# Optimization experiments

Hardware: AMD Instinct MI355X
Metric: run time of the kernel (lower is better)

The kernel has to match this reference:

```python
import jax, jax.numpy as jnp
import numpy as np

BATCH, SEQ, D_IN, D_HID, N_CLS = 256, 128, 1024, 2048, 1024


def setup_inputs() -> dict:
    key = jax.random.key(0)
    ks = jax.random.split(key, 6)
    s_in = 1.0 / np.sqrt(D_IN)
    s_hid = 1.0 / np.sqrt(D_HID)
    return {
        "x": jax.random.normal(ks[0], (BATCH, SEQ, D_IN), dtype=jnp.float32),
        "W_hx": jax.random.normal(ks[1], (D_HID, D_IN), dtype=jnp.float32) * s_in,
        "W_hh": jax.random.normal(ks[2], (D_HID, D_HID), dtype=jnp.float32) * s_hid,
        "W_ph": jax.random.normal(ks[3], (N_CLS, D_HID), dtype=jnp.float32) * s_hid,
        "b_h": jax.random.normal(ks[4], (D_HID,), dtype=jnp.float32) * 0.01,
        "b_p": jax.random.normal(ks[5], (N_CLS,), dtype=jnp.float32) * 0.01,
    }


def reference(x, W_hx, W_hh, W_ph, b_h, b_p):
    # Input projection for all timesteps in one large GEMM: [B,S,Din] @ [Din,H] -> [B,S,H]
    xproj = jnp.einsum("bsd,hd->bsh", x, W_hx) + b_h  # bias folded in once per step
    h0 = jnp.zeros((x.shape[0], W_hh.shape[0]), dtype=x.dtype)

    def step(h_prev, xp_t):
        # h_t = W_hx x_t + W_hh h_prev + b_h (linear recurrence, as in source)
        h_t = xp_t + h_prev @ W_hh.T
        return h_t, None

    # scan over time axis: xproj transposed to [S,B,H]
    h_T, _ = jax.lax.scan(step, h0, jnp.swapaxes(xproj, 0, 1))
    # readout from final hidden state: p = W_ph h_T + b_p -> [B, C]
    p = h_T @ W_ph.T + b_p
    return p
```

## Files before the change

### kernel.cpp

```cpp
#include <hip/hip_runtime.h>
#include <stdint.h>

#define B_SZ   256
#define SEQ_LEN 128
#define DIN    1024
#define DHID   2048
#define NCLS   1024
#define NBLK   256
#define NROUND 8

typedef unsigned short ushort_t;
typedef short bf16x8 __attribute__((ext_vector_type(8)));
typedef float f32x16 __attribute__((ext_vector_type(16)));

__device__ __forceinline__ ushort_t f32_to_bf16(float f) {
  uint32_t u = __builtin_bit_cast(uint32_t, f);
  u = (u + 0x7FFFu + ((u >> 16) & 1u)) >> 16;
  return (ushort_t)u;
}
__device__ __forceinline__ float bf16_to_f32(ushort_t h) {
  uint32_t u = ((uint32_t)h) << 16;
  return __builtin_bit_cast(float, u);
}

__device__ __forceinline__ void llds16(const ushort_t* g, ushort_t* l) {
  __builtin_amdgcn_global_load_lds(
      (const __attribute__((address_space(1))) void*)g,
      (__attribute__((address_space(3))) void*)l, 16, 0, 0);
}

__device__ __forceinline__ void cstore_f32(float* p, float v) {
  __hip_atomic_store(p, v, __ATOMIC_RELAXED, __HIP_MEMORY_SCOPE_AGENT);
}
__device__ __forceinline__ void cstore_u64(void* p, uint64_t v) {
  __hip_atomic_store((uint64_t*)p, v, __ATOMIC_RELAXED, __HIP_MEMORY_SCOPE_AGENT);
}
__device__ __forceinline__ uint64_t cload_u64(const void* p) {
  return __hip_atomic_load((const uint64_t*)p, __ATOMIC_RELAXED, __HIP_MEMORY_SCOPE_AGENT);
}
__device__ __forceinline__ void cstore_u32(unsigned* p, unsigned v) {
  __hip_atomic_store(p, v, __ATOMIC_RELAXED, __HIP_MEMORY_SCOPE_AGENT);
}
__device__ __forceinline__ unsigned cload_u32(const unsigned* p) {
  return __hip_atomic_load(p, __ATOMIC_RELAXED, __HIP_MEMORY_SCOPE_AGENT);
}

__device__ __forceinline__ void gsync(unsigned* flags, unsigned ep) {
  __syncthreads();
  if (threadIdx.x == 0) cstore_u32(&flags[blockIdx.x], ep);
  if (threadIdx.x < 64) {
    const unsigned* f = flags + threadIdx.x * 4;
    for (;;) {
      unsigned a = cload_u32(f + 0), b = cload_u32(f + 1);
      unsigned c = cload_u32(f + 2), d = cload_u32(f + 3);
      bool ok = (a >= ep) & (b >= ep) & (c >= ep) & (d >= ep);
      if (__ballot(ok) == ~0ull) break;
      __builtin_amdgcn_s_sleep(1);
    }
  }
  __syncthreads();
}

__global__ void k_split(const float* __restrict__ s, ushort_t* __restrict__ hi,
                        ushort_t* __restrict__ lo, int n4) {
  int i = blockIdx.x * 256 + threadIdx.x;
  if (i >= n4) return;
  float4 v = ((const float4*)s)[i];
  ushort_t h0 = f32_to_bf16(v.x), h1 = f32_to_bf16(v.y);
  ushort_t h2 = f32_to_bf16(v.z), h3 = f32_to_bf16(v.w);
  ushort4 hv; hv.x = h0; hv.y = h1; hv.z = h2; hv.w = h3;
  ushort4 lv;
  lv.x = f32_to_bf16(v.x - bf16_to_f32(h0));
  lv.y = f32_to_bf16(v.y - bf16_to_f32(h1));
  lv.z = f32_to_bf16(v.z - bf16_to_f32(h2));
  lv.w = f32_to_bf16(v.w - bf16_to_f32(h3));
  ((ushort4*)hi)[i] = hv;
  ((ushort4*)lo)[i] = lv;
}

__global__ void k_cvt(const float* __restrict__ s, ushort_t* __restrict__ d, int n4) {
  int i = blockIdx.x * 256 + threadIdx.x;
  if (i >= n4) return;
  float4 v = ((const float4*)s)[i];
  ushort4 hv;
  hv.x = f32_to_bf16(v.x); hv.y = f32_to_bf16(v.y);
  hv.z = f32_to_bf16(v.z); hv.w = f32_to_bf16(v.w);
  ((ushort4*)d)[i] = hv;
}

__global__ void k_trb(const ushort_t* __restrict__ src, ushort_t* __restrict__ dst) {
  __shared__ ushort_t t[64][65];
  const int bx = blockIdx.x * 64, by = blockIdx.y * 64;
  const int c = threadIdx.x & 63, r0 = (threadIdx.x >> 6) * 16;
#pragma unroll
  for (int i = 0; i < 16; ++i)
    t[r0 + i][c] = src[(size_t)(by + r0 + i) * DHID + bx + c];
  __syncthreads();
#pragma unroll
  for (int i = 0; i < 16; ++i)
    dst[(size_t)(bx + r0 + i) * DHID + by + c] = t[c][r0 + i];
}

__global__ void k_trg(const ushort_t* __restrict__ src, ushort_t* __restrict__ dst,
                      int srcld, int dstld) {
  __shared__ ushort_t t[64][65];
  const int bx = blockIdx.x * 64, by = blockIdx.y * 64;
  const int c = threadIdx.x & 63, r0 = (threadIdx.x >> 6) * 16;
#pragma unroll
  for (int i = 0; i < 16; ++i)
    t[r0 + i][c] = src[(size_t)(by + r0 + i) * srcld + bx + c];
  __syncthreads();
#pragma unroll
  for (int i = 0; i < 16; ++i)
    dst[(size_t)(bx + r0 + i) * dstld + by + c] = t[c][r0 + i];
}

__global__ void k_bvec(const float* __restrict__ W, const float* __restrict__ b,
                       float* __restrict__ out) {
  int row = (blockIdx.x * blockDim.x + threadIdx.x) >> 6;
  int lane = threadIdx.x & 63;
  if (row >= DHID) return;
  float s = 0.0f;
  for (int j = lane; j < DHID; j += 64) s += W[(size_t)row * DHID + j] * b[j];
#pragma unroll
  for (int off = 32; off; off >>= 1) s += __shfl_down(s, off);
  if (lane == 0) out[row] = b[row] + s;
}

struct BigArgs {
  const ushort_t* A[3];
  const ushort_t* B[3];
  int nseg;
  int klen;
  size_t tA, sA;
  size_t ldo;
  const ushort_t* D;
  size_t tD;
  const float* bias;
  ushort_t* out_hi;
  ushort_t* out_lo;
};

__global__ __launch_bounds__(256, 1) void k_big(BigArgs a) {
  __shared__ __align__(16) ushort_t lds[32768];
  const int tid = threadIdx.x, lane = tid & 63, wv = tid >> 6;
  const int l31 = lane & 31, half = lane >> 5;
  const int bm0 = blockIdx.y * 128, bn0 = blockIdx.x * 128;
  const int t_ = bm0 >> 8, mrem = bm0 & 255;
  const int kit = a.klen >> 6;

  f32x16 acc[2][2];
#pragma unroll
  for (int p = 0; p < 2; ++p)
#pragma unroll
    for (int q = 0; q < 2; ++q)
#pragma unroll
      for (int r = 0; r < 16; ++r) acc[p][q][r] = 0.0f;

  auto stage = [&](int buf, int i) {
    int seg = 0, ii = i;
    while (ii >= kit) { ii -= kit; ++seg; }
    const int kc = ii * 64;
    const ushort_t* Ab = a.A[seg];
    const ushort_t* Bb = a.B[seg];
#pragma unroll
    for (int j = 0; j < 4; ++j) {
      int s = tid + 256 * j;
      int prow = s >> 3, glc = (s & 7) ^ (prow & 7);
      llds16(Ab + (size_t)t_ * a.tA + (size_t)(mrem + prow) * a.sA + (kc + glc * 8),
             &lds[(size_t)(buf * 16384 + (wv * 64 + 256 * j) * 16) / 2]);
      llds16(Bb + (size_t)(bn0 + prow) * a.klen + (kc + glc * 8),
             &lds[(size_t)(32768 + buf * 16384 + (wv * 64 + 256 * j) * 16) / 2]);
    }
  };

  const int nit = a.nseg * kit;
  stage(0, 0);
  for (int i = 0; i < nit; ++i) {
    int buf = i & 1;
    if (i + 1 < nit) {
      stage(buf ^ 1, i + 1);
      __builtin_amdgcn_s_waitcnt(0x3FF0 | 8);
    } else {
      __builtin_amdgcn_s_waitcnt(0x3FF0);
    }
    __builtin_amdgcn_s_barrier();
    const ushort_t* At = &lds[buf * 8192];
    const ushort_t* Bt = &lds[16384 + buf * 8192];
#pragma unroll
    for (int ks = 0; ks < 4; ++ks) {
      int ch = ks * 2 + half;
      bf16x8 af[2], bf_[2];
#pragma unroll
      for (int mi = 0; mi < 2; ++mi) {
        int row = (wv & 1) * 64 + mi * 32 + l31;
        int pch = ch ^ (row & 7);
        af[mi] = *(const bf16x8*)&At[row * 64 + pch * 8];
      }
#pragma unroll
      for (int ni = 0; ni < 2; ++ni) {
        int row = (wv >> 1) * 64 + ni * 32 + l31;
        int pch = ch ^ (row & 7);
        bf_[ni] = *(const bf16x8*)&Bt[row * 64 + pch * 8];
      }
#pragma unroll
      for (int mi = 0; mi < 2; ++mi)
#pragma unroll
        for (int ni = 0; ni < 2; ++ni)
          acc[mi][ni] = __builtin_amdgcn_mfma_f32_32x32x16_bf16(
              af[mi], bf_[ni], acc[mi][ni], 0, 0, 0);
    }
    __builtin_amdgcn_s_barrier();
  }

  int gm0 = bm0 + (wv & 1) * 64, gn0 = bn0 + (wv >> 1) * 64;
#pragma unroll
  for (int mi = 0; mi < 2; ++mi)
#pragma unroll
    for (int ni = 0; ni < 2; ++ni)
#pragma unroll
      for (int r = 0; r < 16; ++r) {
        int row = gm0 + mi * 32 + (r & 3) + 8 * (r >> 2) + 4 * half;
        int col = gn0 + ni * 32 + l31;
        float v = acc[mi][ni][r];
        if (a.bias) v += a.bias[col];
        if (a.D)
          v += bf16_to_f32(a.D[(size_t)(row >> 8) * a.tD +
                               (size_t)(row & 255) * 2048 + col]);
        ushort_t hh = f32_to_bf16(v);
        a.out_hi[(size_t)row * a.ldo + col] = hh;
        if (a.out_lo)
          a.out_lo[(size_t)row * a.ldo + col] = f32_to_bf16(v - bf16_to_f32(hh));
      }
}

__global__ __launch_bounds__(512, 2) void k_rnn(
    const ushort_t* __restrict__ w_hi, const ushort_t* __restrict__ w_lo,
    ushort_t* __restrict__ h_hi, ushort_t* __restrict__ h_lo,
    const ushort_t* __restrict__ z_hi, const ushort_t* __restrict__ z_lo,
    float* __restrict__ P, unsigned* __restrict__ flags) {
  __shared__ __align__(16) ushort_t lds[81920];
  char* ldsb = (char*)&lds[0];

  const int tid = threadIdx.x, lane = tid & 63, wv = tid >> 6;
  const int l31 = lane & 31, half = lane >> 5;
  const int kslice = wv & 1, mq = (wv >> 1) & 1, nq = wv >> 2;
  const int b = blockIdx.x;
  const int kb = b & 7, nb = (b >> 3) & 15, mb = b >> 7;
  const int n0 = nb * 128, k0 = kb * 256, m0 = mb * 128;

#pragma unroll
  for (int hl = 0; hl < 2; ++hl) {
    const ushort_t* W = hl ? w_lo : w_hi;
    for (int p = 0; p < 4; ++p)
#pragma unroll
      for (int j = 0; j < 2; ++j) {
        int s = tid + 512 * j;
        int prow = s >> 3, glc = (s & 7) ^ (prow & 7);
        const ushort_t* g = W + (size_t)(n0 + prow) * DHID + (k0 + p * 64 + glc * 8);
        ushort_t* d = (ushort_t*)(ldsb + hl * 65536 + p * 16384 + (wv * 64 + 512 * j) * 16);
        llds16(g, d);
      }
  }
  __builtin_amdgcn_s_waitcnt(0x3FF0);
  __syncthreads();

  const int srow0 = wv * 16 + (lane >> 4);
  const int skk   = 4 * (lane & 15);
  const int sg    = (lane & 15) >> 1;
  const int ssub  = lane & 1;

  uint64_t R[4][4];

  auto regload = [&](int slot, int c) {
    const ushort_t* src = (c < 4) ? h_hi : h_lo;
    const int p = c & 3;
#pragma unroll
    for (int i = 0; i < 4; ++i)
      R[slot][i] = cload_u64(src + (size_t)(m0 + srow0 + 4 * i) * DHID +
                             (k0 + p * 64 + skk));
  };
  auto dswrite = [&](int buf, int slot) {
#pragma unroll
    for (int i = 0; i < 4; ++i) {
      int lr = srow0 + 4 * i;
      *(uint64_t*)(ldsb + 131072 + buf * 16384 + lr * 128 +
                   ((sg ^ (lr & 7)) * 16) + ssub * 8) = R[slot][i];
    }
  };

  auto phaseB = [&](ushort4 zq, ushort4 zl, bool withP) {
    const int r = b;
    const int c0 = tid * 4;
    float v[4] = {bf16_to_f32(zq.x) + bf16_to_f32(zl.x),
                  bf16_to_f32(zq.y) + bf16_to_f32(zl.y),
                  bf16_to_f32(zq.z) + bf16_to_f32(zl.z),
                  bf16_to_f32(zq.w) + bf16_to_f32(zl.w)};
    if (withP) {
#pragma unroll
      for (int k = 0; k < 8; ++k) {
        const float* pp = P + ((size_t)k * B_SZ + r) * DHID + c0;
#pragma unroll
        for (int j = 0; j < 2; ++j) {
          uint64_t q = cload_u64((const uint64_t*)pp + j);
          float2 f = __builtin_bit_cast(float2, q);
          v[2 * j]     += f.x;
          v[2 * j + 1] += f.y;
        }
      }
    }
    ushort_t hh[4], ll[4];
#pragma unroll
    for (int e = 0; e < 4; ++e) {
      hh[e] = f32_to_bf16(v[e]);
      ll[e] = f32_to_bf16(v[e] - bf16_to_f32(hh[e]));
    }
    uint64_t q0, q1;
    __builtin_memcpy(&q0, &hh[0], 8);
    __builtin_memcpy(&q1, &ll[0], 8);
    cstore_u64(h_hi + (size_t)r * DHID + c0, q0);
    cstore_u64(h_lo + (size_t)r * DHID + c0, q1);
  };

  unsigned ep = 1;
  {
    ushort4 zq = *(const ushort4*)(z_hi + (size_t)b * DHID + tid * 4);
    ushort4 zl = *(const ushort4*)(z_lo + (size_t)b * DHID + tid * 4);
    phaseB(zq, zl, false);
  }
  gsync(flags, ep); ++ep;

  for (int j = 1; j < NROUND; ++j) {
    f32x16 acc[2][2];
#pragma unroll
    for (int p = 0; p < 2; ++p)
#pragma unroll
      for (int q = 0; q < 2; ++q)
#pragma unroll
        for (int r = 0; r < 16; ++r) acc[p][q][r] = 0.0f;

    regload(0, 0); regload(1, 1); regload(2, 2); regload(3, 3);
    dswrite(0, 0);
    __syncthreads();

    for (int c = 0; c < 8; ++c) {
      if (c + 4 <= 7) regload(c & 3, c + 4);
      if (c + 1 <= 7) dswrite((c + 1) & 1, (c + 1) & 3);

      const char* At = ldsb + 131072 + (c & 1) * 16384;
      const char* Bh = ldsb + (size_t)(c & 3) * 16384;
      const char* Bl = ldsb + 65536 + (size_t)(c & 3) * 16384;
      const bool isHi = c < 4;
#pragma unroll
      for (int ks = 0; ks < 2; ++ks) {
        const int g = (kslice * 2 + ks) * 2 + half;
        bf16x8 af[2], bh_[2], bl_[2];
#pragma unroll
        for (int mi = 0; mi < 2; ++mi) {
          int row = mq * 64 + mi * 32 + l31;
          af[mi] = *(const bf16x8*)(At + row * 128 + (g ^ (row & 7)) * 16);
        }
#pragma unroll
        for (int ni = 0; ni < 2; ++ni) {
          int row = nq * 64 + ni * 32 + l31;
          int off = row * 128 + (g ^ (row & 7)) * 16;
          bh_[ni] = *(const bf16x8*)(Bh + off);
          if (isHi) bl_[ni] = *(const bf16x8*)(Bl + off);
        }
#pragma unroll
        for (int mi = 0; mi < 2; ++mi)
#pragma unroll
          for (int ni = 0; ni < 2; ++ni) {
            acc[mi][ni] = __builtin_amdgcn_mfma_f32_32x32x16_bf16(
                af[mi], bh_[ni], acc[mi][ni], 0, 0, 0);
            if (isHi)
              acc[mi][ni] = __builtin_amdgcn_mfma_f32_32x32x16_bf16(
                  af[mi], bl_[ni], acc[mi][ni], 0, 0, 0);
          }
      }
      __syncthreads();
    }

    {
      float* scr = (float*)(ldsb + 131072);
      const int pr = mq * 2 + nq;
#pragma unroll
      for (int r = 0; r < 2; ++r) {
        if (kslice == 1) {
#pragma unroll
          for (int ni = 0; ni < 2; ++ni)
#pragma unroll
            for (int reg = 0; reg < 16; ++reg) {
              int row32 = (reg & 3) + 8 * (reg >> 2) + 4 * half;
              scr[pr * 2048 + row32 * 64 + ni * 32 + l31] = acc[r][ni][reg];
            }
        }
        __syncthreads();
        if (kslice == 0) {
#pragma unroll
          for (int ni = 0; ni < 2; ++ni)
#pragma unroll
            for (int reg = 0; reg < 16; ++reg) {
              int row32 = (reg & 3) + 8 * (reg >> 2) + 4 * half;
              acc[r][ni][reg] += scr[pr * 2048 + row32 * 64 + ni * 32 + l31];
            }
        }
        __syncthreads();
      }
    }

    if (kslice == 0) {
      float* Pt = P + (size_t)kb * (B_SZ * DHID);
#pragma unroll
      for (int mi = 0; mi < 2; ++mi)
#pragma unroll
        for (int ni = 0; ni < 2; ++ni)
#pragma unroll
          for (int reg = 0; reg < 16; ++reg) {
            int row = m0 + mq * 64 + mi * 32 + (reg & 3) + 8 * (reg >> 2) + 4 * half;
            int col = n0 + nq * 64 + ni * 32 + l31;
            cstore_f32(&Pt[(size_t)row * DHID + col], acc[mi][ni][reg]);
          }
    }
    ushort4 zq = *(const ushort4*)(z_hi + ((size_t)j * 256 + b) * DHID + tid * 4);
    ushort4 zl = *(const ushort4*)(z_lo + ((size_t)j * 256 + b) * DHID + tid * 4);
    gsync(flags, ep); ++ep;

    phaseB(zq, zl, true);
    gsync(flags, ep); ++ep;
  }
}

struct Seg {
  const ushort_t* A;
  const ushort_t* B;
  int a_stride;
  int b_stride;
  int k_len;
};
struct Args {
  Seg seg[4];
  int n_seg;
  int n_iters;
  const float* bias;
  ushort_t* out_hi;
  ushort_t* out_lo;
  float* out_f32;
  int ldo;
};

#define DEPTH 6
__global__ __launch_bounds__(256, 1) void k_gemm(Args args) {
  __shared__ __align__(16) char pool[DEPTH * 12288];
  const int tid = threadIdx.x, lane = tid & 63, wv = tid >> 6;
  const int bm0 = blockIdx.y * 32, bn0 = blockIdx.x * 64;

  f32x16 acc[2];
#pragma unroll
  for (int c = 0; c < 2; ++c)
#pragma unroll
    for (int r = 0; r < 16; ++r) acc[c][r] = 0.0f;

  const int prow0 = tid >> 3;
  const int glc0 = (tid & 7) ^ (prow0 & 7);
  const int prow1 = (tid + 256) >> 3;
  const int glc1 = (tid & 7) ^ (prow1 & 7);

  auto stage = [&](int buf, const Seg& sg, int k0) {
    const ushort_t* ga = sg.A + (size_t)(bm0 + prow0) * sg.a_stride + (k0 + glc0 * 8);
    const ushort_t* gb0 = sg.B + (size_t)(bn0 + prow0) * sg.b_stride + (k0 + glc0 * 8);
    const ushort_t* gb1 = sg.B + (size_t)(bn0 + prow1) * sg.b_stride + (k0 + glc1 * 8);
    ushort_t* la = (ushort_t*)(pool + buf * 12288) + wv * 512;
    ushort_t* lb = (ushort_t*)(pool + buf * 12288 + 4096) + wv * 512;
    llds16(ga, la);
    llds16(gb0, lb);
    llds16(gb1, lb + 2048);
  };

  const int nit = args.n_iters;
  int sc = 0, kc = 0;
  int nst = nit < (DEPTH - 1) ? nit : (DEPTH - 1);
  for (int s = 0; s < nst; ++s) {
    stage(s, args.seg[sc], kc);
    kc += 64;
    if (kc >= args.seg[sc].k_len) { kc = 0; ++sc; }
  }

  const int half = lane >> 5, l31 = lane & 31;
  const int lch = wv * 2 + half;
  int sb = DEPTH - 1, cb = 0;

  for (int i = 0; i < nit; ++i) {
    int ahead = nit - 1 - i;
    if (ahead > DEPTH - 1) ahead = DEPTH - 1;
    if (i + DEPTH - 1 < nit) {
      stage(sb, args.seg[sc], kc);
      if (++sb == DEPTH) sb = 0;
      kc += 64;
      if (kc >= args.seg[sc].k_len) { kc = 0; ++sc; }
    }
    switch (ahead) {
      case 5: __builtin_amdgcn_s_waitcnt(0x3FF0 | 15); break;
      case 4: __builtin_amdgcn_s_waitcnt(0x3FF0 | 12); break;
      case 3: __builtin_amdgcn_s_waitcnt(0x3FF0 | 9); break;
      case 2: __builtin_amdgcn_s_waitcnt(0x3FF0 | 6); break;
      case 1: __builtin_amdgcn_s_waitcnt(0x3FF0 | 3); break;
      default: __builtin_amdgcn_s_waitcnt(0x3FF0 | 0); break;
    }
    __builtin_amdgcn_s_barrier();

    const ushort_t* tA = (const ushort_t*)(pool + cb * 12288);
    const ushort_t* tB = tA + 2048;
    bf16x8 af, bfm[2];
    {
      int row = l31;
      int pch = lch ^ (row & 7);
      af = *(const bf16x8*)&tA[row * 64 + pch * 8];
    }
#pragma unroll
    for (int ni = 0; ni < 2; ++ni) {
      int row = ni * 32 + l31;
      int pch = lch ^ (row & 7);
      bfm[ni] = *(const bf16x8*)&tB[row * 64 + pch * 8];
    }
#pragma unroll
    for (int ni = 0; ni < 2; ++ni)
      acc[ni] = __builtin_amdgcn_mfma_f32_32x32x16_bf16(af, bfm[ni], acc[ni], 0, 0, 0);

    if (++cb == DEPTH) cb = 0;
    __builtin_amdgcn_s_barrier();
  }

  __syncthreads();
  float* red = (float*)pool + wv * 2048;
#pragma unroll
  for (int ni = 0; ni < 2; ++ni)
#pragma unroll
    for (int r = 0; r < 16; ++r) {
      int row = (r & 3) + 8 * (r >> 2) + 4 * half;
      int col = ni * 32 + l31;
      red[row * 64 + col] = acc[ni][r];
    }
  __syncthreads();

  const float* r0 = (const float*)pool;
  const float* r1 = r0 + 2048;
  const float* r2 = r0 + 4096;
  const float* r3 = r0 + 6144;
#pragma unroll
  for (int j = 0; j < 8; ++j) {
    int e = j * 256 + tid;
    int row = e >> 6, col = e & 63;
    float v = r0[e] + r1[e] + r2[e] + r3[e] + args.bias[bn0 + col];
    size_t o = (size_t)(bm0 + row) * args.ldo + (bn0 + col);
    if (args.out_f32) {
      args.out_f32[o] = v;
    } else {
      ushort_t h = f32_to_bf16(v);
      args.out_hi[o] = h;
      args.out_lo[o] = f32_to_bf16(v - bf16_to_f32(h));
    }
  }
}

extern "C" void kernel_launch(void* const* d_in, const int* in_sizes, int n_in,
                              void* d_out, int out_size, void* d_ws, size_t ws_size,
                              hipStream_t stream) {
  const float* x   = (const float*)d_in[0];
  const float* Whx = (const float*)d_in[1];
  const float* Whh = (const float*)d_in[2];
  const float* Wph = (const float*)d_in[3];
  const float* bh  = (const float*)d_in[4];
  const float* bp  = (const float*)d_in[5];

  const size_t WSZ = (size_t)DHID * DHID * 2;
  char* p = (char*)d_ws;
  ushort_t* whh_hi = (ushort_t*)p; p += WSZ;
  ushort_t* whh_lo = (ushort_t*)p; p += WSZ;
  ushort_t* whhT_hi= (ushort_t*)p; p += WSZ;
  ushort_t* whhT_lo= (ushort_t*)p; p += WSZ;
  ushort_t* w2_hi  = (ushort_t*)p; p += WSZ;
  ushort_t* w2_lo  = (ushort_t*)p; p += WSZ;
  ushort_t* w4_hi  = (ushort_t*)p; p += WSZ;
  ushort_t* w4_lo  = (ushort_t*)p; p += WSZ;
  ushort_t* w8_hi  = (ushort_t*)p; p += WSZ;
  ushort_t* w8_lo  = (ushort_t*)p; p += WSZ;
  ushort_t* w16_hi = (ushort_t*)p; p += WSZ;
  ushort_t* w16_lo = (ushort_t*)p; p += WSZ;
  ushort_t* wT_hi  = (ushort_t*)p; p += WSZ;
  ushort_t* wT_lo  = (ushort_t*)p; p += WSZ;
  ushort_t* whx_b  = (ushort_t*)p; p += (size_t)DHID * DIN * 2;
  ushort_t* whxT   = (ushort_t*)p; p += (size_t)DIN * DHID * 2;
  ushort_t* wa_b   = (ushort_t*)p; p += (size_t)DHID * DIN * 2;
  ushort_t* wph_b  = (ushort_t*)p; p += (size_t)NCLS * DHID * 2;
  ushort_t* x_b    = (ushort_t*)p; p += (size_t)B_SZ * SEQ_LEN * DIN * 2;
  ushort_t* z2_b   = (ushort_t*)p; p += (size_t)64 * B_SZ * DHID * 2;
  ushort_t* z4_b   = (ushort_t*)p; p += (size_t)32 * B_SZ * DHID * 2;
  ushort_t* z8_b   = (ushort_t*)p; p += (size_t)16 * B_SZ * DHID * 2;
  ushort_t* z8_lo  = (ushort_t*)p; p += (size_t)16 * B_SZ * DHID * 2;
  ushort_t* z16_b  = (ushort_t*)p; p += (size_t)8 * B_SZ * DHID * 2;
  ushort_t* z16_lo = (ushort_t*)p; p += (size_t)8 * B_SZ * DHID * 2;
  float*    Part   = (float*)p;    p += (size_t)8 * B_SZ * DHID * 4;
  ushort_t* h_hi   = (ushort_t*)p; p += (size_t)B_SZ * DHID * 2;
  ushort_t* h_lo   = (ushort_t*)p; p += (size_t)B_SZ * DHID * 2;
  float*    b2_ws  = (float*)p;    p += (size_t)DHID * 4;
  unsigned* flags  = (unsigned*)p; p += NBLK * 4;

  hipMemsetAsync(flags, 0, NBLK * 4, stream);

  {
    int n4 = DHID * DHID / 4;
    k_split<<<(n4 + 255) / 256, 256, 0, stream>>>(Whh, whh_hi, whh_lo, n4);
  }
  k_trb<<<dim3(32, 32), 256, 0, stream>>>(whh_hi, whhT_hi);
  k_trb<<<dim3(32, 32), 256, 0, stream>>>(whh_lo, whhT_lo);
  {
    int n4 = DHID * DIN / 4;
    k_cvt<<<(n4 + 255) / 256, 256, 0, stream>>>(Whx, whx_b, n4);
  }
  {
    int n4 = NCLS * DHID / 4;
    k_cvt<<<(n4 + 255) / 256, 256, 0, stream>>>(Wph, wph_b, n4);
  }
  {
    int n4 = B_SZ * SEQ_LEN * DIN / 4;
    k_cvt<<<(n4 + 255) / 256, 256, 0, stream>>>(x, x_b, n4);
  }
  k_trg<<<dim3(DIN / 64, DHID / 64), 256, 0, stream>>>(whx_b, whxT, DIN, DHID);
  k_bvec<<<512, 256, 0, stream>>>(Whh, bh, b2_ws);

  const size_t TBLK = (size_t)512 * DHID;

  {
    BigArgs a = {};
    a.A[0] = whh_hi; a.B[0] = whxT;
    a.A[1] = whh_lo; a.B[1] = whxT;
    a.nseg = 2; a.klen = DHID; a.tA = (size_t)256 * DHID; a.sA = DHID;
    a.ldo = DIN; a.out_hi = wa_b;
    k_big<<<dim3(DIN / 128, DHID / 128), 256, 0, stream>>>(a);
  }
  {
    BigArgs a = {};
    a.A[0] = whh_hi; a.B[0] = whhT_hi;
    a.A[1] = whh_hi; a.B[1] = whhT_lo;
    a.A[2] = whh_lo; a.B[2] = whhT_hi;
    a.nseg = 3; a.klen = DHID; a.tA = (size_t)256 * DHID; a.sA = DHID;
    a.ldo = 2048; a.out_hi = w2_hi; a.out_lo = w2_lo;
    k_big<<<dim3(16, 16), 256, 0, stream>>>(a);
  }
  {
    BigArgs a = {};
    a.A[0] = x_b;       a.B[0] = wa_b;
    a.A[1] = x_b + DIN; a.B[1] = whx_b;
    a.nseg = 2; a.klen = DIN;
    a.tA = (size_t)2 * DIN; a.sA = (size_t)SEQ_LEN * DIN;
    a.ldo = 2048; a.bias = b2_ws; a.out_hi = z2_b;
    k_big<<<dim3(16, 128), 256, 0, stream>>>(a);
  }
  k_trb<<<dim3(32, 32), 256, 0, stream>>>(w2_hi, wT_hi);
  k_trb<<<dim3(32, 32), 256, 0, stream>>>(w2_lo, wT_lo);
  {
    BigArgs a = {};
    a.A[0] = w2_hi; a.B[0] = wT_hi;
    a.A[1] = w2_hi; a.B[1] = wT_lo;
    a.A[2] = w2_lo; a.B[2] = wT_hi;
    a.nseg = 3; a.klen = DHID; a.tA = (size_t)256 * DHID; a.sA = DHID;
    a.ldo = 2048; a.out_hi = w4_hi; a.out_lo = w4_lo;
    k_big<<<dim3(16, 16), 256, 0, stream>>>(a);
  }
  {
    BigArgs a = {};
    a.A[0] = z2_b; a.B[0] = w2_hi; a.nseg = 1; a.klen = DHID;
    a.tA = TBLK; a.sA = DHID;
    a.D = z2_b + (size_t)256 * DHID; a.tD = TBLK;
    a.ldo = 2048; a.out_hi = z4_b;
    k_big<<<dim3(16, 64), 256, 0, stream>>>(a);
  }
  k_trb<<<dim3(32, 32), 256, 0, stream>>>(w4_hi, wT_hi);
  k_trb<<<dim3(32, 32), 256, 0, stream>>>(w4_lo, wT_lo);
  {
    BigArgs a = {};
    a.A[0] = w4_hi; a.B[0] = wT_hi;
    a.A[1] = w4_hi; a.B[1] = wT_lo;
    a.A[2] = w4_lo; a.B[2] = wT_hi;
    a.nseg = 3; a.klen = DHID; a.tA = (size_t)256 * DHID; a.sA = DHID;
    a.ldo = 2048; a.out_hi = w8_hi; a.out_lo = w8_lo;
    k_big<<<dim3(16, 16), 256, 0, stream>>>(a);
  }
  {
    BigArgs a = {};
    a.A[0] = z4_b; a.B[0] = w4_hi; a.nseg = 1; a.klen = DHID;
    a.tA = TBLK; a.sA = DHID;
    a.D = z4_b + (size_t)256 * DHID; a.tD = TBLK;
    a.ldo = 2048; a.out_hi = z8_b; a.out_lo = z8_lo;
    k_big<<<dim3(16, 32), 256, 0, stream>>>(a);
  }
  k_trb<<<dim3(32, 32), 256, 0, stream>>>(w8_hi, wT_hi);
  k_trb<<<dim3(32, 32), 256, 0, stream>>>(w8_lo, wT_lo);
  {
    BigArgs a = {};
    a.A[0] = w8_hi; a.B[0] = wT_hi;
    a.A[1] = w8_hi; a.B[1] = wT_lo;
    a.A[2] = w8_lo; a.B[2] = wT_hi;
    a.nseg = 3; a.klen = DHID; a.tA = (size_t)256 * DHID; a.sA = DHID;
    a.ldo = 2048; a.out_hi = w16_hi; a.out_lo = w16_lo;
    k_big<<<dim3(16, 16), 256, 0, stream>>>(a);
  }
  {
    BigArgs a = {};
    a.A[0] = z8_b;  a.B[0] = w8_hi;
    a.A[1] = z8_b;  a.B[1] = w8_lo;
    a.A[2] = z8_lo; a.B[2] = w8_hi;
    a.nseg = 3; a.klen = DHID; a.tA = TBLK; a.sA = DHID;
    a.D = z8_b + (size_t)256 * DHID; a.tD = TBLK;
    a.ldo = 2048; a.out_hi = z16_b; a.out_lo = z16_lo;
    k_big<<<dim3(16, 16), 256, 0, stream>>>(a);
  }

  k_rnn<<<dim3(NBLK), 512, 0, stream>>>(w16_hi, w16_lo, h_hi, h_lo,
                                        z16_b, z16_lo, Part, flags);

  {
    Args a = {};
    a.seg[0] = { h_hi, wph_b, DHID, DHID, DHID };
    a.seg[1] = { h_lo, wph_b, DHID, DHID, DHID };
    a.n_seg = 2; a.n_iters = 2 * DHID / 64;
    a.bias = bp; a.out_hi = nullptr; a.out_lo = nullptr;
    a.out_f32 = (float*)d_out; a.ldo = NCLS;
    k_gemm<<<dim3(NCLS / 64, B_SZ / 32), 256, 0, stream>>>(a);
  }
}
```

Before: 1.124 ms.

## Merge independent GEMM launches, remap blocks across XCDs, store x time-major

Pairs independent GEMMs (the W-power squaring and the z-level reduction) into single k_big launches over a 1D grid. Each launch picks its argument set by block index and applies an XCD-aware remapping of block IDs. The x conversion now writes a time-major [S,B,D] layout so z2 A-tiles read contiguous rows. The intent is fewer launches, better CU fill for small 256-block GEMMs, and better L2 locality per XCD. The risk is the extra indexing logic and possible load imbalance between the paired GEMMs.

```diff
diff --git a/kernel.cpp b/kernel.cpp
--- a/kernel.cpp
+++ b/kernel.cpp
@@ -12,6 +12,7 @@
 typedef unsigned short ushort_t;
 typedef short bf16x8 __attribute__((ext_vector_type(8)));
 typedef float f32x16 __attribute__((ext_vector_type(16)));
+typedef ushort_t u16x8 __attribute__((ext_vector_type(8)));
 
 __device__ __forceinline__ ushort_t f32_to_bf16(float f) {
   uint32_t u = __builtin_bit_cast(uint32_t, f);
@@ -88,6 +89,23 @@
   ((ushort4*)d)[i] = hv;
 }
 
+__global__ void k_cvtT(const float* __restrict__ s, ushort_t* __restrict__ d) {
+  int i = blockIdx.x * 256 + threadIdx.x;
+  int dd = (i & (DIN / 8 - 1)) * 8;
+  int bs = i >> 7;
+  int b = bs >> 7;
+  int t = bs & (SEQ_LEN - 1);
+  const float* src = s + (size_t)bs * DIN + dd;
+  float4 v0 = *(const float4*)src;
+  float4 v1 = *(const float4*)(src + 4);
+  u16x8 hv;
+  hv[0] = f32_to_bf16(v0.x); hv[1] = f32_to_bf16(v0.y);
+  hv[2] = f32_to_bf16(v0.z); hv[3] = f32_to_bf16(v0.w);
+  hv[4] = f32_to_bf16(v1.x); hv[5] = f32_to_bf16(v1.y);
+  hv[6] = f32_to_bf16(v1.z); hv[7] = f32_to_bf16(v1.w);
+  *(u16x8*)(d + ((size_t)t * B_SZ + b) * DIN + dd) = hv;
+}
+
 __global__ void k_trb(const ushort_t* __restrict__ src, ushort_t* __restrict__ dst) {
   __shared__ ushort_t t[64][65];
   const int bx = blockIdx.x * 64, by = blockIdx.y * 64;
@@ -139,13 +157,21 @@
   const float* bias;
   ushort_t* out_hi;
   ushort_t* out_lo;
+  int lognx;
 };
 
-__global__ __launch_bounds__(256, 1) void k_big(BigArgs a) {
+__global__ __launch_bounds__(256, 1) void k_big(BigArgs a0, BigArgs a1, int nblk0) {
   __shared__ __align__(16) ushort_t lds[32768];
   const int tid = threadIdx.x, lane = tid & 63, wv = tid >> 6;
   const int l31 = lane & 31, half = lane >> 5;
-  const int bm0 = blockIdx.y * 128, bn0 = blockIdx.x * 128;
+
+  const int cpx = gridDim.x >> 3;
+  int wg = (blockIdx.x & 7) * cpx + (blockIdx.x >> 3);
+  const BigArgs& a = (wg < nblk0) ? a0 : a1;
+  if (wg >= nblk0) wg -= nblk0;
+
+  const int bn0 = (wg & ((1 << a.lognx) - 1)) * 128;
+  const int bm0 = (wg >> a.lognx) * 128;
   const int t_ = bm0 >> 8, mrem = bm0 & 255;
   const int kit = a.klen >> 6;
 
@@ -593,7 +619,7 @@
   ushort_t* whxT   = (ushort_t*)p; p += (size_t)DIN * DHID * 2;
   ushort_t* wa_b   = (ushort_t*)p; p += (size_t)DHID * DIN * 2;
   ushort_t* wph_b  = (ushort_t*)p; p += (size_t)NCLS * DHID * 2;
-  ushort_t* x_b    = (ushort_t*)p; p += (size_t)B_SZ * SEQ_LEN * DIN * 2;
+  ushort_t* xT     = (ushort_t*)p; p += (size_t)B_SZ * SEQ_LEN * DIN * 2;
   ushort_t* z2_b   = (ushort_t*)p; p += (size_t)64 * B_SZ * DHID * 2;
   ushort_t* z4_b   = (ushort_t*)p; p += (size_t)32 * B_SZ * DHID * 2;
   ushort_t* z8_b   = (ushort_t*)p; p += (size_t)16 * B_SZ * DHID * 2;
@@ -622,100 +648,84 @@
     int n4 = NCLS * DHID / 4;
     k_cvt<<<(n4 + 255) / 256, 256, 0, stream>>>(Wph, wph_b, n4);
   }
-  {
-    int n4 = B_SZ * SEQ_LEN * DIN / 4;
-    k_cvt<<<(n4 + 255) / 256, 256, 0, stream>>>(x, x_b, n4);
-  }
+  k_cvtT<<<(B_SZ * SEQ_LEN * DIN / 8) / 256, 256, 0, stream>>>(x, xT);
   k_trg<<<dim3(DIN / 64, DHID / 64), 256, 0, stream>>>(whx_b, whxT, DIN, DHID);
   k_bvec<<<512, 256, 0, stream>>>(Whh, bh, b2_ws);
 
   const size_t TBLK = (size_t)512 * DHID;
 
-  {
-    BigArgs a = {};
-    a.A[0] = whh_hi; a.B[0] = whxT;
-    a.A[1] = whh_lo; a.B[1] = whxT;
-    a.nseg = 2; a.klen = DHID; a.tA = (size_t)256 * DHID; a.sA = DHID;
-    a.ldo = DIN; a.out_hi = wa_b;
-    k_big<<<dim3(DIN / 128, DHID / 128), 256, 0, stream>>>(a);
-  }
-  {
-    BigArgs a = {};
-    a.A[0] = whh_hi; a.B[0] = whhT_hi;
-    a.A[1] = whh_hi; a.B[1] = whhT_lo;
-    a.A[2] = whh_lo; a.B[2] = whhT_hi;
-    a.nseg = 3; a.klen = DHID; a.tA = (size_t)256 * DHID; a.sA = DHID;
-    a.ldo = 2048; a.out_hi = w2_hi; a.out_lo = w2_lo;
-    k_big<<<dim3(16, 16), 256, 0, stream>>>(a);
-  }
-  {
-    BigArgs a = {};
-    a.A[0] = x_b;       a.B[0] = wa_b;
-    a.A[1] = x_b + DIN; a.B[1] = whx_b;
-    a.nseg = 2; a.klen = DIN;
-    a.tA = (size_t)2 * DIN; a.sA = (size_t)SEQ_LEN * DIN;
-    a.ldo = 2048; a.bias = b2_ws; a.out_hi = z2_b;
-    k_big<<<dim3(16, 128), 256, 0, stream>>>(a);
-  }
+  BigArgs aWa = {};
+  aWa.A[0] = whh_hi; aWa.B[0] = whxT;
+  aWa.A[1] = whh_lo; aWa.B[1] = whxT;
+  aWa.nseg = 2; aWa.klen = DHID; aWa.tA = (size_t)256 * DHID; aWa.sA = DHID;
+  aWa.ldo = DIN; aWa.out_hi = wa_b; aWa.lognx = 3;
+
+  BigArgs aW2 = {};
+  aW2.A[0] = whh_hi; aW2.B[0] = whhT_hi;
+  aW2.A[1] = whh_hi; aW2.B[1] = whhT_lo;
+  aW2.A[2] = whh_lo; aW2.B[2] = whhT_hi;
+  aW2.nseg = 3; aW2.klen = DHID; aW2.tA = (size_t)256 * DHID; aW2.sA = DHID;
+  aW2.ldo = 2048; aW2.out_hi = w2_hi; aW2.out_lo = w2_lo; aW2.lognx = 4;
+
+  BigArgs az2 = {};
+  az2.A[0] = xT;              az2.B[0] = wa_b;
+  az2.A[1] = xT + (size_t)B_SZ * DIN; az2.B[1] = whx_b;
+  az2.nseg = 2; az2.klen = DIN;
+  az2.tA = (size_t)2 * B_SZ * DIN; az2.sA = DIN;
+  az2.ldo = 2048; az2.bias = b2_ws; az2.out_hi = z2_b; az2.lognx = 4;
+
+  BigArgs aW4 = {};
+  aW4.A[0] = w2_hi; aW4.B[0] = wT_hi;
+  aW4.A[1] = w2_hi; aW4.B[1] = wT_lo;
+  aW4.A[2] = w2_lo; aW4.B[2] = wT_hi;
+  aW4.nseg = 3; aW4.klen = DHID; aW4.tA = (size_t)256 * DHID; aW4.sA = DHID;
+  aW4.ldo = 2048; aW4.out_hi = w4_hi; aW4.out_lo = w4_lo; aW4.lognx = 4;
+
+  BigArgs az4 = {};
+  az4.A[0] = z2_b; az4.B[0] = w2_hi; az4.nseg = 1; az4.klen = DHID;
+  az4.tA = TBLK; az4.sA = DHID;
+  az4.D = z2_b + (size_t)256 * DHID; az4.tD = TBLK;
+  az4.ldo = 2048; az4.out_hi = z4_b; az4.lognx = 4;
+
+  BigArgs aW8 = {};
+  aW8.A[0] = w4_hi; aW8.B[0] = wT_hi;
+  aW8.A[1] = w4_hi; aW8.B[1] = wT_lo;
+  aW8.A[2] = w4_lo; aW8.B[2] = wT_hi;
+  aW8.nseg = 3; aW8.klen = DHID; aW8.tA = (size_t)256 * DHID; aW8.sA = DHID;
+  aW8.ldo = 2048; aW8.out_hi = w8_hi; aW8.out_lo = w8_lo; aW8.lognx = 4;
+
+  BigArgs az8 = {};
+  az8.A[0] = z4_b; az8.B[0] = w4_hi; az8.nseg = 1; az8.klen = DHID;
+  az8.tA = TBLK; az8.sA = DHID;
+  az8.D = z4_b + (size_t)256 * DHID; az8.tD = TBLK;
+  az8.ldo = 2048; az8.out_hi = z8_b; az8.out_lo = z8_lo; az8.lognx = 4;
+
+  BigArgs aW16 = {};
+  aW16.A[0] = w8_hi; aW16.B[0] = wT_hi;
+  aW16.A[1] = w8_hi; aW16.B[1] = wT_lo;
+  aW16.A[2] = w8_lo; aW16.B[2] = wT_hi;
+  aW16.nseg = 3; aW16.klen = DHID; aW16.tA = (size_t)256 * DHID; aW16.sA = DHID;
+  aW16.ldo = 2048; aW16.out_hi = w16_hi; aW16.out_lo = w16_lo; aW16.lognx = 4;
+
+  BigArgs az16 = {};
+  az16.A[0] = z8_b;  az16.B[0] = w8_hi;
+  az16.A[1] = z8_b;  az16.B[1] = w8_lo;
+  az16.A[2] = z8_lo; az16.B[2] = w8_hi;
+  az16.nseg = 3; az16.klen = DHID; az16.tA = TBLK; az16.sA = DHID;
+  az16.D = z8_b + (size_t)256 * DHID; az16.tD = TBLK;
+  az16.ldo = 2048; az16.out_hi = z16_b; az16.out_lo = z16_lo; az16.lognx = 4;
+
+  k_big<<<dim3(384), 256, 0, stream>>>(aWa, aW2, 128);
+  k_big<<<dim3(2048), 256, 0, stream>>>(az2, az2, 2048);
   k_trb<<<dim3(32, 32), 256, 0, stream>>>(w2_hi, wT_hi);
   k_trb<<<dim3(32, 32), 256, 0, stream>>>(w2_lo, wT_lo);
-  {
-    BigArgs a = {};
-    a.A[0] = w2_hi; a.B[0] = wT_hi;
-    a.A[1] = w2_hi; a.B[1] = wT_lo;
-    a.A[2] = w2_lo; a.B[2] = wT_hi;
-    a.nseg = 3; a.klen = DHID; a.tA = (size_t)256 * DHID; a.sA = DHID;
-    a.ldo = 2048; a.out_hi = w4_hi; a.out_lo = w4_lo;
-    k_big<<<dim3(16, 16), 256, 0, stream>>>(a);
-  }
-  {
-    BigArgs a = {};
-    a.A[0] = z2_b; a.B[0] = w2_hi; a.nseg = 1; a.klen = DHID;
-    a.tA = TBLK; a.sA = DHID;
-    a.D = z2_b + (size_t)256 * DHID; a.tD = TBLK;
-    a.ldo = 2048; a.out_hi = z4_b;
-    k_big<<<dim3(16, 64), 256, 0, stream>>>(a);
-  }
+  k_big<<<dim3(1280), 256, 0, stream>>>(aW4, az4, 256);
   k_trb<<<dim3(32, 32), 256, 0, stream>>>(w4_hi, wT_hi);
   k_trb<<<dim3(32, 32), 256, 0, stream>>>(w4_lo, wT_lo);
-  {
-    BigArgs a = {};
-    a.A[0] = w4_hi; a.B[0] = wT_hi;
-    a.A[1] = w4_hi; a.B[1] = wT_lo;
-    a.A[2] = w4_lo; a.B[2] = wT_hi;
-    a.nseg = 3; a.klen = DHID; a.tA = (size_t)256 * DHID; a.sA = DHID;
-    a.ldo = 2048; a.out_hi = w8_hi; a.out_lo = w8_lo;
-    k_big<<<dim3(16, 16), 256, 0, stream>>>(a);
-  }
-  {
-    BigArgs a = {};
-    a.A[0] = z4_b; a.B[0] = w4_hi; a.nseg = 1; a.klen = DHID;
-    a.tA = TBLK; a.sA = DHID;
-    a.D = z4_b + (size_t)256 * DHID; a.tD = TBLK;
-    a.ldo = 2048; a.out_hi = z8_b; a.out_lo = z8_lo;
-    k_big<<<dim3(16, 32), 256, 0, stream>>>(a);
-  }
+  k_big<<<dim3(768), 256, 0, stream>>>(aW8, az8, 256);
   k_trb<<<dim3(32, 32), 256, 0, stream>>>(w8_hi, wT_hi);
   k_trb<<<dim3(32, 32), 256, 0, stream>>>(w8_lo, wT_lo);
-  {
-    BigArgs a = {};
-    a.A[0] = w8_hi; a.B[0] = wT_hi;
-    a.A[1] = w8_hi; a.B[1] = wT_lo;
-    a.A[2] = w8_lo; a.B[2] = wT_hi;
-    a.nseg = 3; a.klen = DHID; a.tA = (size_t)256 * DHID; a.sA = DHID;
-    a.ldo = 2048; a.out_hi = w16_hi; a.out_lo = w16_lo;
-    k_big<<<dim3(16, 16), 256, 0, stream>>>(a);
-  }
-  {
-    BigArgs a = {};
-    a.A[0] = z8_b;  a.B[0] = w8_hi;
-    a.A[1] = z8_b;  a.B[1] = w8_lo;
-    a.A[2] = z8_lo; a.B[2] = w8_hi;
-    a.nseg = 3; a.klen = DHID; a.tA = TBLK; a.sA = DHID;
-    a.D = z8_b + (size_t)256 * DHID; a.tD = TBLK;
-    a.ldo = 2048; a.out_hi = z16_b; a.out_lo = z16_lo;
-    k_big<<<dim3(16, 16), 256, 0, stream>>>(a);
-  }
+  k_big<<<dim3(512), 256, 0, stream>>>(aW16, az16, 256);
 
   k_rnn<<<dim3(NBLK), 512, 0, stream>>>(w16_hi, w16_lo, h_hi, h_lo,
                                         z16_b, z16_lo, Part, flags);
```

Result: slower. 1.975 ms (+75.7%).
